# Performance work log

Hardware: AMD Instinct MI355X
Metric: run time of the kernel (lower is better)

The kernel has to match this reference:

```python
import jax, jax.numpy as jnp
import numpy as np
from jax import lax

B, J, I = 32, 48, 48          # batch, target len, source len
W = 2                          # target_window_size
CTX = 2 * W + 1                # 5
E, H = 128, 256                # embedding_size, hidden_units
VT, VS = 32000, 32000          # target / source vocab
S = 2 * J                      # HMM states (word + null)


def setup_inputs() -> dict:
    key = jax.random.key(0)
    ks = jax.random.split(key, 12)
    inp = {
        "target_embedding": jax.random.normal(ks[0], (VT, E), jnp.float32) * 0.02,
        "W_bridge": jax.random.normal(ks[1], (E * CTX, E), jnp.float32) * 0.02,
        "W_hidden": jax.random.normal(ks[2], (E, H), jnp.float32) * 0.02,
        "b_hidden": jnp.zeros((H,), jnp.float32),
        "W_vocab": jax.random.normal(ks[3], (H, VS), jnp.float32) * 0.02,
        "b_vocab": jnp.zeros((VS,), jnp.float32),
        "transition": jax.random.uniform(ks[4], (B, S, S), jnp.float32, 0.01, 1.0),
        "initial_transition": jax.random.uniform(ks[5], (B, S), jnp.float32, 0.01, 1.0),
        "targets_ctx": jax.random.randint(ks[6], (B, J * CTX), 0, VT, jnp.int32),
        "targets_ctx_null": jax.random.randint(ks[7], (B, J * CTX), 0, VT, jnp.int32),
        "sources": jax.random.randint(ks[8], (B, I), 0, VS, jnp.int32),
    }
    return inp


def _emission(emb, Wb, Wh, bh, Wv, bv, ctx_ids, sources):
    # embedding lookup + context reshape: [B, J*CTX, E] -> [B, J, CTX*E]
    x = emb[ctx_ids].reshape(ctx_ids.shape[0], -1, CTX * E)
    h = jnp.tanh(jnp.einsum('bjc,ce,eh->bjh', x, Wb, Wh) + bh)  # bridge+hidden
    probs = jax.nn.softmax(h @ Wv + bv, axis=-1)                # [B, J, VS]
    # per-example gather of source token columns -> [B, J, I]
    return jax.vmap(lambda p, s: p[:, s])(probs, sources)


def _forward_backward(pi, A, em):
    # pi [B,S], A [B,S,S], em [B,S,I]; scaled HMM forward-backward
    e = jnp.moveaxis(em, 2, 0)  # [I, B, S]
    a0 = pi * e[0]
    c0 = a0.sum(-1, keepdims=True)
    a0 = a0 / c0

    def fstep(a, ei):
        an = jnp.einsum('bs,bst->bt', a, A) * ei
        c = an.sum(-1, keepdims=True)
        an = an / c
        return an, (an, c)

    _, (alphas, cs) = lax.scan(fstep, a0, e[1:])
    alphas = jnp.concatenate([a0[None], alphas], 0)          # [I,B,S]
    cs = jnp.concatenate([c0[None], cs], 0)                  # [I,B,1]

    def bstep(b, inp):
        ei, ci = inp
        bn = jnp.einsum('bst,bt->bs', A, ei * b) / ci
        return bn, bn

    bI = jnp.ones_like(a0)
    _, betas_rev = lax.scan(bstep, bI, (e[1:][::-1], cs[1:][::-1]))
    betas = jnp.concatenate([betas_rev[::-1], bI[None]], 0)  # [I,B,S]

    gamma = alphas * betas                                   # state posteriors
    loglik = jnp.log(cs[..., 0]).sum(0)                      # [B]
    return jnp.moveaxis(gamma, 0, 2), loglik


def reference(target_embedding, W_bridge, W_hidden, b_hidden, W_vocab, b_vocab,
              transition, initial_transition, targets_ctx, targets_ctx_null, sources):
    em_word = _emission(target_embedding, W_bridge, W_hidden, b_hidden,
                        W_vocab, b_vocab, targets_ctx, sources)       # [B,J,I]
    em_null = _emission(target_embedding, W_bridge, W_hidden, b_hidden,
                        W_vocab, b_vocab, targets_ctx_null, sources)  # [B,J,I]
    emission = jnp.concatenate([em_word, em_null], axis=1)            # [B,2J,I]
    gamma, loglik = _forward_backward(initial_transition, transition, emission)
    return gamma, -loglik
```

## Files before the change

kernel.cpp:

```cpp
#include <hip/hip_runtime.h>
#include <hip/hip_bf16.h>

#define NB 32
#define NJ 48
#define NI 48
#define NCTX 5
#define NE 128
#define NH 256
#define NVS 32000
#define NS 96
#define NR 3072

typedef __attribute__((ext_vector_type(8))) short bf16x8;
typedef __attribute__((ext_vector_type(4))) float f32x4;

__device__ __forceinline__ unsigned short f2b(float f) {
  __hip_bfloat16 h = __float2bfloat16(f);
  return *reinterpret_cast<unsigned short*>(&h);
}
__device__ __forceinline__ float wave_sum(float v) {
  v += __shfl_xor(v, 1);
  v += __shfl_xor(v, 2);
  v += __shfl_xor(v, 4);
  v += __shfl_xor(v, 8);
  v += __shfl_xor(v, 16);
  v += __shfl_xor(v, 32);
  return v;
}
__device__ __forceinline__ void gload_lds16(const void* g, void* l) {
  __builtin_amdgcn_global_load_lds(
      (const __attribute__((address_space(1))) void*)g,
      (__attribute__((address_space(3))) void*)l, 16, 0, 0);
}

__global__ __launch_bounds__(256) void k_transpose(const float* __restrict__ Wv,
                                                   unsigned char* __restrict__ Wv8) {
  __shared__ float tile[64][65];
  int t = threadIdx.x;
  int v0 = blockIdx.x * 64, k0 = blockIdx.y * 64;
  {
    int kr = t >> 4, vq = t & 15;
#pragma unroll
    for (int it = 0; it < 4; ++it) {
      float4 v = *(const float4*)&Wv[(k0 + kr + 16 * it) * NVS + v0 + vq * 4];
      tile[kr + 16 * it][vq * 4 + 0] = v.x;
      tile[kr + 16 * it][vq * 4 + 1] = v.y;
      tile[kr + 16 * it][vq * 4 + 2] = v.z;
      tile[kr + 16 * it][vq * 4 + 3] = v.w;
    }
  }
  __syncthreads();
  {
    int vl = t >> 2, kq = t & 3;
    unsigned int q8[4];
#pragma unroll
    for (int d = 0; d < 4; ++d) {
      float f0 = tile[kq * 16 + d * 4 + 0][vl] * 64.0f;
      float f1 = tile[kq * 16 + d * 4 + 1][vl] * 64.0f;
      float f2 = tile[kq * 16 + d * 4 + 2][vl] * 64.0f;
      float f3 = tile[kq * 16 + d * 4 + 3][vl] * 64.0f;
      int w = __builtin_amdgcn_cvt_pk_fp8_f32(f0, f1, 0, false);
      w = __builtin_amdgcn_cvt_pk_fp8_f32(f2, f3, w, true);
      q8[d] = (unsigned int)w;
    }
    *(uint4*)&Wv8[(v0 + vl) * 256 + k0 + kq * 16] = *(uint4*)q8;
  }
}

__global__ __launch_bounds__(256) void k_t2b(const float* __restrict__ src,
                                             unsigned short* __restrict__ dst,
                                             int R, int C) {
  __shared__ float tile[64][65];
  int t = threadIdx.x;
  int r0 = blockIdx.x * 64, c0 = blockIdx.y * 64;
  {
    int rr = t >> 4, cq = t & 15;
#pragma unroll
    for (int it = 0; it < 4; ++it) {
      float4 v = *(const float4*)&src[(r0 + rr + 16 * it) * C + c0 + cq * 4];
      tile[rr + 16 * it][cq * 4 + 0] = v.x;
      tile[rr + 16 * it][cq * 4 + 1] = v.y;
      tile[rr + 16 * it][cq * 4 + 2] = v.z;
      tile[rr + 16 * it][cq * 4 + 3] = v.w;
    }
  }
  __syncthreads();
  {
    int cc = t >> 2, rq = t & 3;
    unsigned short pk[16];
#pragma unroll
    for (int q = 0; q < 16; ++q) pk[q] = f2b(tile[rq * 16 + q][cc]);
    *(uint4*)&dst[(c0 + cc) * R + r0 + rq * 16] = *(uint4*)&pk[0];
    *(uint4*)&dst[(c0 + cc) * R + r0 + rq * 16 + 8] = *(uint4*)&pk[8];
  }
}

__global__ __launch_bounds__(256) void k_xb(const float* __restrict__ emb,
                                            const unsigned short* __restrict__ Wbt,
                                            const int* __restrict__ tc, const int* __restrict__ tcn,
                                            unsigned short* __restrict__ xb) {
  __shared__ unsigned short Ax[64 * 72];
  __shared__ unsigned short Bw[128 * 72];
  __shared__ unsigned short xout[64 * 136];
  int t = threadIdx.x;
  int r0 = blockIdx.x * 64;
  int wave = t >> 6, lane = t & 63;
  int wm = wave >> 1, wn = wave & 1;
  int lg = lane >> 4, lr = lane & 15;
  int arow = t >> 2, aseg = t & 3;
  int r = r0 + arow;
  int half = r / 1536, rem = r % 1536, bb = rem / 48, jj = rem % 48;
  const int* ids = half ? tcn : tc;
  int brow = t >> 1, bseg = t & 1;

  f32x4 acc[2][4];
#pragma unroll
  for (int m = 0; m < 2; ++m)
#pragma unroll
    for (int n = 0; n < 4; ++n) acc[m][n] = (f32x4){0.f, 0.f, 0.f, 0.f};

  for (int step = 0; step < 10; ++step) {
    int k0 = step * 64;
    int p = k0 >> 7;
    int e0 = k0 & 127;
    {
      int id = ids[bb * 240 + jj * 5 + p];
      const float4* er = (const float4*)&emb[id * 128 + e0 + aseg * 16];
      unsigned short pk[16];
#pragma unroll
      for (int q = 0; q < 4; ++q) {
        float4 v = er[q];
        pk[q * 4 + 0] = f2b(v.x);
        pk[q * 4 + 1] = f2b(v.y);
        pk[q * 4 + 2] = f2b(v.z);
        pk[q * 4 + 3] = f2b(v.w);
      }
      *(uint4*)&Ax[arow * 72 + aseg * 16] = *(uint4*)&pk[0];
      *(uint4*)&Ax[arow * 72 + aseg * 16 + 8] = *(uint4*)&pk[8];
    }
    {
      const uint4* wp = (const uint4*)&Wbt[brow * 640 + k0 + bseg * 32];
      uint4* dp = (uint4*)&Bw[brow * 72 + bseg * 32];
      uint4 w0 = wp[0], w1 = wp[1], w2 = wp[2], w3 = wp[3];
      dp[0] = w0; dp[1] = w1; dp[2] = w2; dp[3] = w3;
    }
    __syncthreads();
#pragma unroll
    for (int kk = 0; kk < 2; ++kk) {
      bf16x8 a[2], b[4];
#pragma unroll
      for (int m = 0; m < 2; ++m)
        a[m] = *(const bf16x8*)&Ax[(wm * 32 + m * 16 + lr) * 72 + kk * 32 + lg * 8];
#pragma unroll
      for (int n = 0; n < 4; ++n)
        b[n] = *(const bf16x8*)&Bw[(wn * 64 + n * 16 + lr) * 72 + kk * 32 + lg * 8];
#pragma unroll
      for (int m = 0; m < 2; ++m)
#pragma unroll
        for (int n = 0; n < 4; ++n)
          acc[m][n] = __builtin_amdgcn_mfma_f32_16x16x32_bf16(a[m], b[n], acc[m][n], 0, 0, 0);
    }
    __syncthreads();
  }
#pragma unroll
  for (int m = 0; m < 2; ++m)
#pragma unroll
    for (int n = 0; n < 4; ++n)
#pragma unroll
      for (int g = 0; g < 4; ++g)
        xout[(wm * 32 + m * 16 + lg * 4 + g) * 136 + wn * 64 + n * 16 + lr] = f2b(acc[m][n][g]);
  __syncthreads();
  {
    int orow = t >> 2, os = t & 3;
#pragma unroll
    for (int i = 0; i < 4; ++i)
      ((uint4*)&xb[(r0 + orow) * 128])[os * 4 + i] = *(uint4*)&xout[orow * 136 + (os * 4 + i) * 8];
  }
}

__global__ __launch_bounds__(256) void k_h(const unsigned short* __restrict__ xb,
                                           const unsigned short* __restrict__ Wht,
                                           const float* __restrict__ bh,
                                           unsigned char* __restrict__ hb8) {
  __shared__ char smem[69632];
  unsigned short* Asm = (unsigned short*)smem;
  unsigned short* Bsm = (unsigned short*)(smem + 34816);
  unsigned char* o8 = (unsigned char*)smem;
  int t = threadIdx.x;
  int r0 = blockIdx.x * 128, n0 = blockIdx.y * 128;
  int wave = t >> 6, lane = t & 63;
  int wm = wave >> 1, wn = wave & 1;
  int lg = lane >> 4, lr = lane & 15;
  {
    int row = t >> 1, seg = t & 1;
#pragma unroll
    for (int i = 0; i < 8; ++i) {
      *(uint4*)&Asm[row * 136 + seg * 64 + i * 8] = *(const uint4*)&xb[(r0 + row) * 128 + seg * 64 + i * 8];
      *(uint4*)&Bsm[row * 136 + seg * 64 + i * 8] = *(const uint4*)&Wht[(n0 + row) * 128 + seg * 64 + i * 8];
    }
  }
  __syncthreads();
  f32x4 acc[4][4];
#pragma unroll
  for (int m = 0; m < 4; ++m)
#pragma unroll
    for (int n = 0; n < 4; ++n) acc[m][n] = (f32x4){0.f, 0.f, 0.f, 0.f};
#pragma unroll
  for (int kk = 0; kk < 4; ++kk) {
    bf16x8 a[4], b[4];
#pragma unroll
    for (int m = 0; m < 4; ++m)
      a[m] = *(const bf16x8*)&Asm[(wm * 64 + m * 16 + lr) * 136 + kk * 32 + lg * 8];
#pragma unroll
    for (int n = 0; n < 4; ++n)
      b[n] = *(const bf16x8*)&Bsm[(wn * 64 + n * 16 + lr) * 136 + kk * 32 + lg * 8];
#pragma unroll
    for (int m = 0; m < 4; ++m)
#pragma unroll
      for (int n = 0; n < 4; ++n)
        acc[m][n] = __builtin_amdgcn_mfma_f32_16x16x32_bf16(a[m], b[n], acc[m][n], 0, 0, 0);
  }
  __syncthreads();
#pragma unroll
  for (int n = 0; n < 4; ++n) {
    int cl = wn * 64 + n * 16 + lr;
    float bvv = bh[n0 + cl];
#pragma unroll
    for (int m = 0; m < 4; ++m) {
#pragma unroll
      for (int g = 0; g < 4; ++g) {
        int rl = wm * 64 + m * 16 + lg * 4 + g;
        float hv = tanhf(acc[m][n][g] + bvv);
        int p8 = __builtin_amdgcn_cvt_pk_fp8_f32(hv * 256.0f, 0.0f, 0, false);
        o8[rl * 144 + cl] = (unsigned char)(p8 & 0xFF);
      }
    }
  }
  __syncthreads();
  {
    int row = t >> 1, seg = t & 1;
#pragma unroll
    for (int i = 0; i < 4; ++i)
      *(uint4*)&hb8[(r0 + row) * 256 + n0 + seg * 64 + i * 16] = *(uint4*)&o8[row * 144 + seg * 64 + i * 16];
  }
}

__global__ __launch_bounds__(256) void k_denom(const unsigned char* __restrict__ hb8,
                                               const unsigned char* __restrict__ Wv8,
                                               const float* __restrict__ bv,
                                               float* __restrict__ dpart) {
  __shared__ __align__(16) char smem[65536];
  unsigned char* Asm = (unsigned char*)smem;
  unsigned char* Bsm = (unsigned char*)(smem + 32768);
  float* red2 = (float*)smem;
  int t = threadIdx.x;
  int bid = blockIdx.x;
  int xcd = bid & 7;
  int pos = bid >> 3;
  int tile = xcd * 750 + pos;
  int vt = tile / 24, rt = tile % 24;
  int v0 = vt * 128, r0 = rt * 128;
  int wave = t >> 6, lane = t & 63;
  int wm = wave >> 1, wn = wave & 1;
  int lg = lane >> 4, lr = lane & 15;

  {
    int rloc = lane >> 4;
    int seg = lane & 15;
#pragma unroll
    for (int c = 0; c < 8; ++c) {
      int chunk = wave * 8 + c;
      int row = chunk * 4 + rloc;
      int gseg = seg ^ (row & 15);
      gload_lds16(&hb8[(r0 + row) * 256 + gseg * 16], &Asm[chunk * 1024]);
      gload_lds16(&Wv8[(v0 + row) * 256 + gseg * 16], &Bsm[chunk * 1024]);
    }
  }
  __syncthreads();

  f32x4 acc[4][4];
#pragma unroll
  for (int m = 0; m < 4; ++m)
#pragma unroll
    for (int n = 0; n < 4; ++n) acc[m][n] = (f32x4){0.f, 0.f, 0.f, 0.f};

#pragma unroll
  for (int K = 0; K < 4; ++K) {
#pragma unroll
    for (int kk = 0; kk < 2; ++kk) {
      int lseg = (K << 2) + (kk << 1) + (lg >> 1);
      int hb = (lg & 1) << 3;
      long long a[4], b[4];
#pragma unroll
      for (int m = 0; m < 4; ++m) {
        int rr = wm * 64 + m * 16 + lr;
        a[m] = *(const long long*)&Asm[rr * 256 + ((lseg ^ lr) << 4) + hb];
      }
#pragma unroll
      for (int n = 0; n < 4; ++n) {
        int rr = wn * 64 + n * 16 + lr;
        b[n] = *(const long long*)&Bsm[rr * 256 + ((lseg ^ lr) << 4) + hb];
      }
#pragma unroll
      for (int m = 0; m < 4; ++m)
#pragma unroll
        for (int n = 0; n < 4; ++n)
          acc[m][n] = __builtin_amdgcn_mfma_f32_16x16x32_fp8_fp8(a[m], b[n], acc[m][n], 0, 0, 0);
    }
  }

  const float SC = 6.103515625e-05f;
  float rs[4][4];
#pragma unroll
  for (int m = 0; m < 4; ++m)
#pragma unroll
    for (int g = 0; g < 4; ++g) rs[m][g] = 0.f;
#pragma unroll
  for (int m = 0; m < 4; ++m) {
#pragma unroll
    for (int n = 0; n < 4; ++n) {
      float bvv = bv[v0 + wn * 64 + n * 16 + lr];
#pragma unroll
      for (int g = 0; g < 4; ++g) rs[m][g] += __expf(acc[m][n][g] * SC + bvv);
    }
  }
#pragma unroll
  for (int m = 0; m < 4; ++m)
#pragma unroll
    for (int g = 0; g < 4; ++g) {
      float v = rs[m][g];
      v += __shfl_xor(v, 1);
      v += __shfl_xor(v, 2);
      v += __shfl_xor(v, 4);
      v += __shfl_xor(v, 8);
      rs[m][g] = v;
    }
  __syncthreads();
  if (lr == 0) {
#pragma unroll
    for (int m = 0; m < 4; ++m)
#pragma unroll
      for (int g = 0; g < 4; ++g)
        red2[wn * 128 + wm * 64 + m * 16 + lg * 4 + g] = rs[m][g];
  }
  __syncthreads();
  if (t < 128) dpart[vt * NR + r0 + t] = red2[t] + red2[128 + t];
}

__global__ void k_reduce(const float* __restrict__ dpart, float* __restrict__ dsum) {
  int r = blockIdx.x * 256 + threadIdx.x;
  float s = 0.f;
  for (int vt = 0; vt < 250; ++vt) s += dpart[vt * NR + r];
  dsum[r] = s;
}

__global__ __launch_bounds__(64) void k_emis(const unsigned char* __restrict__ hb8,
                                             const unsigned char* __restrict__ Wv8,
                                             const float* __restrict__ bv,
                                             const float* __restrict__ dsum,
                                             const int* __restrict__ src,
                                             float* __restrict__ em) {
  __shared__ unsigned char A8[48 * 256];
  __shared__ unsigned char B8[48 * 256];
  int t = threadIdx.x;
  int bh = blockIdx.x;
  int b = bh & 31, half = bh >> 5;
  int row4 = t >> 4, seg = t & 15;
  int rbase = half * 1536 + b * 48;
#pragma unroll
  for (int c = 0; c < 12; ++c) {
    int row = c * 4 + row4;
    int gseg = seg ^ (row & 15);
    gload_lds16(&hb8[(rbase + row) * 256 + gseg * 16], &A8[c * 1024]);
    int sv = src[b * 48 + row];
    gload_lds16(&Wv8[sv * 256 + gseg * 16], &B8[c * 1024]);
  }
  __syncthreads();
  int lg = t >> 4, lr = t & 15;
  f32x4 acc[3][3];
#pragma unroll
  for (int m = 0; m < 3; ++m)
#pragma unroll
    for (int n = 0; n < 3; ++n) acc[m][n] = (f32x4){0.f, 0.f, 0.f, 0.f};
#pragma unroll
  for (int kk = 0; kk < 8; ++kk) {
    long long a[3], bb[3];
#pragma unroll
    for (int m = 0; m < 3; ++m) {
      int rr = m * 16 + lr;
      int off = rr * 256 + ((((kk << 1) | (lg >> 1)) ^ (rr & 15)) << 4) + ((lg & 1) << 3);
      a[m] = *(const long long*)&A8[off];
      bb[m] = *(const long long*)&B8[off];
    }
#pragma unroll
    for (int m = 0; m < 3; ++m)
#pragma unroll
      for (int n = 0; n < 3; ++n)
        acc[m][n] = __builtin_amdgcn_mfma_f32_16x16x32_fp8_fp8(a[m], bb[n], acc[m][n], 0, 0, 0);
  }
  const float SC = 6.103515625e-05f;
#pragma unroll
  for (int n = 0; n < 3; ++n) {
    int i = n * 16 + lr;
    int sv = src[b * 48 + i];
    float bvv = bv[sv];
#pragma unroll
    for (int m = 0; m < 3; ++m) {
#pragma unroll
      for (int g = 0; g < 4; ++g) {
        int j = m * 16 + lg * 4 + g;
        float val = __expf(acc[m][n][g] * SC + bvv) / dsum[rbase + j];
        em[b * 4608 + (half * 48 + j) * 48 + i] = val;
      }
    }
  }
}

__global__ __launch_bounds__(192) void k_fb(const float* __restrict__ Atr, const float* __restrict__ pi,
                                            const float* __restrict__ em, float* __restrict__ alph,
                                            float* __restrict__ betas, float* __restrict__ out1) {
  __shared__ float A_st[96 * 97];
  __shared__ float em_lds[48 * 97];
  __shared__ __align__(16) float vec_lds[96];
  __shared__ float red[3];
  int t = threadIdx.x;
  int bid = blockIdx.x;
  int b = bid & 31;
  int role = bid >> 5;
  int col = t >> 1, half = t & 1;
  int base = b * 4608;

  for (int idx = t; idx < 96 * 96; idx += 192) {
    int s = idx / 96, tt = idx % 96;
    A_st[s * 97 + tt] = Atr[b * 9216 + idx];
  }
  for (int idx = t; idx < 96 * 48; idx += 192) {
    int s = idx / 48, i = idx % 48;
    em_lds[i * 97 + s] = em[base + idx];
  }
  __syncthreads();

  float Areg[48];
  if (role == 0) {
#pragma unroll
    for (int ss = 0; ss < 48; ++ss) Areg[ss] = A_st[(half * 48 + ss) * 97 + col];

    float llsum;
    {
      float v = pi[b * 96 + col] * em_lds[0 * 97 + col];
      float ws = half ? 0.f : v;
      ws = wave_sum(ws);
      if ((t & 63) == 0) red[t >> 6] = ws;
      __syncthreads();
      float c = red[0] + red[1] + red[2];
      float a = v / c;
      if (!half) {
        vec_lds[col] = a;
        alph[base + col] = a;
      }
      llsum = logf(c);
      __syncthreads();
    }
    for (int i = 1; i < 48; ++i) {
      float p = 0.f;
      const float4* ap = (const float4*)&vec_lds[half * 48];
#pragma unroll
      for (int q = 0; q < 12; ++q) {
        float4 av = ap[q];
        p += av.x * Areg[4 * q] + av.y * Areg[4 * q + 1] + av.z * Areg[4 * q + 2] + av.w * Areg[4 * q + 3];
      }
      p += __shfl_xor(p, 1);
      float an = p * em_lds[i * 97 + col];
      float ws = half ? 0.f : an;
      ws = wave_sum(ws);
      if ((t & 63) == 0) red[t >> 6] = ws;
      __syncthreads();
      float c = red[0] + red[1] + red[2];
      float a = an / c;
      if (!half) {
        vec_lds[col] = a;
        alph[base + i * 96 + col] = a;
      }
      llsum += logf(c);
      __syncthreads();
    }
    if (t == 0) out1[b] = -llsum;
  } else {
#pragma unroll
    for (int tt = 0; tt < 48; ++tt) Areg[tt] = A_st[col * 97 + half * 48 + tt];

    if (!half) {
      betas[base + 47 * 96 + col] = 1.0f;
      vec_lds[col] = em_lds[47 * 97 + col];
    }
    __syncthreads();
    for (int i = 46; i >= 0; --i) {
      float p = 0.f;
      const float4* ep = (const float4*)&vec_lds[half * 48];
#pragma unroll
      for (int q = 0; q < 12; ++q) {
        float4 ev = ep[q];
        p += ev.x * Areg[4 * q] + ev.y * Areg[4 * q + 1] + ev.z * Areg[4 * q + 2] + ev.w * Areg[4 * q + 3];
      }
      p += __shfl_xor(p, 1);
      float ws = half ? 0.f : p;
      ws = wave_sum(ws);
      if ((t & 63) == 0) red[t >> 6] = ws;
      __syncthreads();
      float c = red[0] + red[1] + red[2];
      float bt = p / c;
      if (!half) {
        betas[base + i * 96 + col] = bt;
        vec_lds[col] = em_lds[i * 97 + col] * bt;
      }
      __syncthreads();
    }
  }
}

__global__ __launch_bounds__(128) void k_gamma(const float* __restrict__ alph,
                                               const float* __restrict__ betas,
                                               float* __restrict__ out0) {
  __shared__ float red[2];
  int b = blockIdx.x, i = blockIdx.y;
  int t = threadIdx.x;
  float g = 0.f;
  if (t < 96) g = alph[b * 4608 + i * 96 + t] * betas[b * 4608 + i * 96 + t];
  float ws = wave_sum(g);
  if ((t & 63) == 0) red[t >> 6] = ws;
  __syncthreads();
  float c = red[0] + red[1];
  if (t < 96) out0[b * 4608 + t * 48 + i] = g / c;
}

extern "C" void kernel_launch(void* const* d_in, const int* in_sizes, int n_in,
                              void* d_out, int out_size, void* d_ws, size_t ws_size,
                              hipStream_t stream) {
  const float* emb = (const float*)d_in[0];
  const float* Wb  = (const float*)d_in[1];
  const float* Wh  = (const float*)d_in[2];
  const float* bh  = (const float*)d_in[3];
  const float* Wv  = (const float*)d_in[4];
  const float* bv  = (const float*)d_in[5];
  const float* Atr = (const float*)d_in[6];
  const float* pi  = (const float*)d_in[7];
  const int* tc    = (const int*)d_in[8];
  const int* tcn   = (const int*)d_in[9];
  const int* src   = (const int*)d_in[10];

  float* out0 = (float*)d_out;
  float* out1 = out0 + NB * NS * NI;

  char* ws = (char*)d_ws;
  unsigned char* wv8 = (unsigned char*)(ws);
  unsigned char* hb8 = (unsigned char*)(ws + 8192000);
  float* dpart       = (float*)(ws + 8978432);
  float* betas       = (float*)(ws + 8978432);
  float* dsum        = (float*)(ws + 12050432);
  float* em          = (float*)(ws + 12062720);
  float* alph        = (float*)(ws + 12652544);
  unsigned short* wbt = (unsigned short*)(ws + 13242368);
  unsigned short* wht = (unsigned short*)(ws + 13406208);
  unsigned short* xb  = (unsigned short*)(ws + 13471744);

  k_transpose<<<dim3(500, 4), 256, 0, stream>>>(Wv, wv8);
  k_t2b<<<dim3(10, 2), 256, 0, stream>>>(Wb, wbt, 640, 128);
  k_t2b<<<dim3(2, 4), 256, 0, stream>>>(Wh, wht, 128, 256);
  k_xb<<<48, 256, 0, stream>>>(emb, wbt, tc, tcn, xb);
  k_h<<<dim3(24, 2), 256, 0, stream>>>(xb, wht, bh, hb8);
  k_denom<<<6000, 256, 0, stream>>>(hb8, wv8, bv, dpart);
  k_reduce<<<12, 256, 0, stream>>>(dpart, dsum);
  k_emis<<<64, 64, 0, stream>>>(hb8, wv8, bv, dsum, src, em);
  k_fb<<<64, 192, 0, stream>>>(Atr, pi, em, alph, betas, out1);
  k_gamma<<<dim3(32, 48), 128, 0, stream>>>(alph, betas, out0);
}
```

Measured before the change: 161.6 us.

## Double-buffer Wv tiles in k_denom covering two vocab tiles per block; shrink k_xb tiles

k_denom now has each block process two 128-column vocab tiles for one row tile. The A operand stays resident in LDS and the Wv operand streams in 64-byte K slices through a double buffer, with the next slice prefetched during MFMA work. The aim is to halve A reloads, cut LDS use for better occupancy, and overlap global loads with compute, at the cost of one barrier per K step. Separately, k_xb switches to 32-row tiles and twice as many blocks to spread the small GEMM over more CUs.

```diff
diff --git a/kernel.cpp b/kernel.cpp
--- a/kernel.cpp
+++ b/kernel.cpp
@@ -99,44 +99,36 @@
                                             const unsigned short* __restrict__ Wbt,
                                             const int* __restrict__ tc, const int* __restrict__ tcn,
                                             unsigned short* __restrict__ xb) {
-  __shared__ unsigned short Ax[64 * 72];
+  __shared__ unsigned short Ax[32 * 72];
   __shared__ unsigned short Bw[128 * 72];
-  __shared__ unsigned short xout[64 * 136];
-  int t = threadIdx.x;
-  int r0 = blockIdx.x * 64;
+  __shared__ unsigned short xout[32 * 136];
+  int t = threadIdx.x;
+  int r0 = blockIdx.x * 32;
   int wave = t >> 6, lane = t & 63;
   int wm = wave >> 1, wn = wave & 1;
   int lg = lane >> 4, lr = lane & 15;
-  int arow = t >> 2, aseg = t & 3;
+  int arow = t >> 3, aseg = t & 7;
   int r = r0 + arow;
   int half = r / 1536, rem = r % 1536, bb = rem / 48, jj = rem % 48;
   const int* ids = half ? tcn : tc;
   int brow = t >> 1, bseg = t & 1;
 
-  f32x4 acc[2][4];
-#pragma unroll
-  for (int m = 0; m < 2; ++m)
-#pragma unroll
-    for (int n = 0; n < 4; ++n) acc[m][n] = (f32x4){0.f, 0.f, 0.f, 0.f};
+  f32x4 acc[4];
+#pragma unroll
+  for (int n = 0; n < 4; ++n) acc[n] = (f32x4){0.f, 0.f, 0.f, 0.f};
 
   for (int step = 0; step < 10; ++step) {
     int k0 = step * 64;
-    int p = k0 >> 7;
-    int e0 = k0 & 127;
+    int p = step >> 1;
+    int e0 = (step & 1) * 64;
     {
       int id = ids[bb * 240 + jj * 5 + p];
-      const float4* er = (const float4*)&emb[id * 128 + e0 + aseg * 16];
-      unsigned short pk[16];
-#pragma unroll
-      for (int q = 0; q < 4; ++q) {
-        float4 v = er[q];
-        pk[q * 4 + 0] = f2b(v.x);
-        pk[q * 4 + 1] = f2b(v.y);
-        pk[q * 4 + 2] = f2b(v.z);
-        pk[q * 4 + 3] = f2b(v.w);
-      }
-      *(uint4*)&Ax[arow * 72 + aseg * 16] = *(uint4*)&pk[0];
-      *(uint4*)&Ax[arow * 72 + aseg * 16 + 8] = *(uint4*)&pk[8];
+      const float4* er = (const float4*)&emb[id * 128 + e0 + aseg * 8];
+      float4 v0 = er[0], v1 = er[1];
+      unsigned short pk[8];
+      pk[0] = f2b(v0.x); pk[1] = f2b(v0.y); pk[2] = f2b(v0.z); pk[3] = f2b(v0.w);
+      pk[4] = f2b(v1.x); pk[5] = f2b(v1.y); pk[6] = f2b(v1.z); pk[7] = f2b(v1.w);
+      *(uint4*)&Ax[arow * 72 + aseg * 8] = *(uint4*)&pk[0];
     }
     {
       const uint4* wp = (const uint4*)&Wbt[brow * 640 + k0 + bseg * 32];
@@ -147,34 +139,25 @@
     __syncthreads();
 #pragma unroll
     for (int kk = 0; kk < 2; ++kk) {
-      bf16x8 a[2], b[4];
-#pragma unroll
-      for (int m = 0; m < 2; ++m)
-        a[m] = *(const bf16x8*)&Ax[(wm * 32 + m * 16 + lr) * 72 + kk * 32 + lg * 8];
-#pragma unroll
-      for (int n = 0; n < 4; ++n)
-        b[n] = *(const bf16x8*)&Bw[(wn * 64 + n * 16 + lr) * 72 + kk * 32 + lg * 8];
-#pragma unroll
-      for (int m = 0; m < 2; ++m)
-#pragma unroll
-        for (int n = 0; n < 4; ++n)
-          acc[m][n] = __builtin_amdgcn_mfma_f32_16x16x32_bf16(a[m], b[n], acc[m][n], 0, 0, 0);
+      bf16x8 a = *(const bf16x8*)&Ax[(wm * 16 + lr) * 72 + kk * 32 + lg * 8];
+#pragma unroll
+      for (int n = 0; n < 4; ++n) {
+        bf16x8 b = *(const bf16x8*)&Bw[(wn * 64 + n * 16 + lr) * 72 + kk * 32 + lg * 8];
+        acc[n] = __builtin_amdgcn_mfma_f32_16x16x32_bf16(a, b, acc[n], 0, 0, 0);
+      }
     }
     __syncthreads();
   }
 #pragma unroll
-  for (int m = 0; m < 2; ++m)
-#pragma unroll
-    for (int n = 0; n < 4; ++n)
-#pragma unroll
-      for (int g = 0; g < 4; ++g)
-        xout[(wm * 32 + m * 16 + lg * 4 + g) * 136 + wn * 64 + n * 16 + lr] = f2b(acc[m][n][g]);
-  __syncthreads();
-  {
-    int orow = t >> 2, os = t & 3;
-#pragma unroll
-    for (int i = 0; i < 4; ++i)
-      ((uint4*)&xb[(r0 + orow) * 128])[os * 4 + i] = *(uint4*)&xout[orow * 136 + (os * 4 + i) * 8];
+  for (int n = 0; n < 4; ++n)
+#pragma unroll
+    for (int g = 0; g < 4; ++g)
+      xout[(wm * 16 + lg * 4 + g) * 136 + wn * 64 + n * 16 + lr] = f2b(acc[n][g]);
+  __syncthreads();
+  {
+    int orow = t >> 3, os = t & 7;
+    *(uint4*)&xb[(r0 + orow) * 128 + os * 16] = *(uint4*)&xout[orow * 136 + os * 16];
+    *(uint4*)&xb[(r0 + orow) * 128 + os * 16 + 8] = *(uint4*)&xout[orow * 136 + os * 16 + 8];
   }
 }
 
@@ -249,35 +232,41 @@
                                                const unsigned char* __restrict__ Wv8,
                                                const float* __restrict__ bv,
                                                float* __restrict__ dpart) {
-  __shared__ __align__(16) char smem[65536];
-  unsigned char* Asm = (unsigned char*)smem;
-  unsigned char* Bsm = (unsigned char*)(smem + 32768);
-  float* red2 = (float*)smem;
+  __shared__ __align__(16) unsigned char Asm[32768];
+  __shared__ __align__(16) unsigned char Bsm[2][8192];
+  __shared__ float red2[2][128];
   int t = threadIdx.x;
   int bid = blockIdx.x;
   int xcd = bid & 7;
   int pos = bid >> 3;
-  int tile = xcd * 750 + pos;
-  int vt = tile / 24, rt = tile % 24;
-  int v0 = vt * 128, r0 = rt * 128;
+  int tile = xcd * 375 + pos;
+  int vtp = tile / 24, rt = tile % 24;
+  int r0 = rt * 128;
   int wave = t >> 6, lane = t & 63;
   int wm = wave >> 1, wn = wave & 1;
   int lg = lane >> 4, lr = lane & 15;
 
   {
-    int rloc = lane >> 4;
-    int seg = lane & 15;
+    int rloc = lane >> 4, seg = lane & 15;
 #pragma unroll
     for (int c = 0; c < 8; ++c) {
       int chunk = wave * 8 + c;
       int row = chunk * 4 + rloc;
       int gseg = seg ^ (row & 15);
       gload_lds16(&hb8[(r0 + row) * 256 + gseg * 16], &Asm[chunk * 1024]);
-      gload_lds16(&Wv8[(v0 + row) * 256 + gseg * 16], &Bsm[chunk * 1024]);
-    }
-  }
-  __syncthreads();
-
+    }
+  }
+  int brloc = lane >> 2, bseg = lane & 3;
+#pragma unroll
+  for (int c = 0; c < 2; ++c) {
+    int i = wave * 2 + c;
+    int row = i * 16 + brloc;
+    int gseg = bseg ^ ((row >> 1) & 3);
+    gload_lds16(&Wv8[(vtp * 256 + row) * 256 + 0 * 64 + gseg * 16], &Bsm[0][i * 1024]);
+  }
+  __syncthreads();
+
+  const float SC = 6.103515625e-05f;
   f32x4 acc[4][4];
 #pragma unroll
   for (int m = 0; m < 4; ++m)
@@ -285,21 +274,35 @@
     for (int n = 0; n < 4; ++n) acc[m][n] = (f32x4){0.f, 0.f, 0.f, 0.f};
 
 #pragma unroll
-  for (int K = 0; K < 4; ++K) {
+  for (int step = 0; step < 8; ++step) {
+    int vt = step >> 2, ks = step & 3, buf = step & 1;
+    if (step < 7) {
+      int ns = step + 1;
+      int nvt = ns >> 2, nks = ns & 3, nbuf = ns & 1;
+#pragma unroll
+      for (int c = 0; c < 2; ++c) {
+        int i = wave * 2 + c;
+        int row = i * 16 + brloc;
+        int gseg = bseg ^ ((row >> 1) & 3);
+        gload_lds16(&Wv8[((vtp * 2 + nvt) * 128 + row) * 256 + nks * 64 + gseg * 16],
+                    &Bsm[nbuf][i * 1024]);
+      }
+    }
 #pragma unroll
     for (int kk = 0; kk < 2; ++kk) {
-      int lseg = (K << 2) + (kk << 1) + (lg >> 1);
+      int lsa = ks * 4 + kk * 2 + (lg >> 1);
+      int sb = kk * 2 + (lg >> 1);
       int hb = (lg & 1) << 3;
       long long a[4], b[4];
 #pragma unroll
       for (int m = 0; m < 4; ++m) {
         int rr = wm * 64 + m * 16 + lr;
-        a[m] = *(const long long*)&Asm[rr * 256 + ((lseg ^ lr) << 4) + hb];
+        a[m] = *(const long long*)&Asm[rr * 256 + ((lsa ^ lr) << 4) + hb];
       }
 #pragma unroll
       for (int n = 0; n < 4; ++n) {
         int rr = wn * 64 + n * 16 + lr;
-        b[n] = *(const long long*)&Bsm[rr * 256 + ((lseg ^ lr) << 4) + hb];
+        b[n] = *(const long long*)&Bsm[buf][rr * 64 + ((sb ^ ((rr >> 1) & 3)) << 4) + hb];
       }
 #pragma unroll
       for (int m = 0; m < 4; ++m)
@@ -307,44 +310,47 @@
         for (int n = 0; n < 4; ++n)
           acc[m][n] = __builtin_amdgcn_mfma_f32_16x16x32_fp8_fp8(a[m], b[n], acc[m][n], 0, 0, 0);
     }
-  }
-
-  const float SC = 6.103515625e-05f;
-  float rs[4][4];
-#pragma unroll
-  for (int m = 0; m < 4; ++m)
-#pragma unroll
-    for (int g = 0; g < 4; ++g) rs[m][g] = 0.f;
-#pragma unroll
-  for (int m = 0; m < 4; ++m) {
-#pragma unroll
-    for (int n = 0; n < 4; ++n) {
-      float bvv = bv[v0 + wn * 64 + n * 16 + lr];
-#pragma unroll
-      for (int g = 0; g < 4; ++g) rs[m][g] += __expf(acc[m][n][g] * SC + bvv);
-    }
-  }
-#pragma unroll
-  for (int m = 0; m < 4; ++m)
-#pragma unroll
-    for (int g = 0; g < 4; ++g) {
-      float v = rs[m][g];
-      v += __shfl_xor(v, 1);
-      v += __shfl_xor(v, 2);
-      v += __shfl_xor(v, 4);
-      v += __shfl_xor(v, 8);
-      rs[m][g] = v;
-    }
-  __syncthreads();
-  if (lr == 0) {
-#pragma unroll
-    for (int m = 0; m < 4; ++m)
-#pragma unroll
-      for (int g = 0; g < 4; ++g)
-        red2[wn * 128 + wm * 64 + m * 16 + lg * 4 + g] = rs[m][g];
-  }
-  __syncthreads();
-  if (t < 128) dpart[vt * NR + r0 + t] = red2[t] + red2[128 + t];
+    if (ks == 3) {
+      int v0 = (vtp * 2 + vt) * 128;
+      float rs[4][4];
+#pragma unroll
+      for (int m = 0; m < 4; ++m)
+#pragma unroll
+        for (int g = 0; g < 4; ++g) rs[m][g] = 0.f;
+#pragma unroll
+      for (int m = 0; m < 4; ++m) {
+#pragma unroll
+        for (int n = 0; n < 4; ++n) {
+          float bvv = bv[v0 + wn * 64 + n * 16 + lr];
+#pragma unroll
+          for (int g = 0; g < 4; ++g) rs[m][g] += __expf(acc[m][n][g] * SC + bvv);
+          acc[m][n] = (f32x4){0.f, 0.f, 0.f, 0.f};
+        }
+      }
+#pragma unroll
+      for (int m = 0; m < 4; ++m)
+#pragma unroll
+        for (int g = 0; g < 4; ++g) {
+          float v = rs[m][g];
+          v += __shfl_xor(v, 1);
+          v += __shfl_xor(v, 2);
+          v += __shfl_xor(v, 4);
+          v += __shfl_xor(v, 8);
+          rs[m][g] = v;
+        }
+      if (lr == 0) {
+#pragma unroll
+        for (int m = 0; m < 4; ++m)
+#pragma unroll
+          for (int g = 0; g < 4; ++g)
+            red2[wn][wm * 64 + m * 16 + lg * 4 + g] = rs[m][g];
+      }
+      __syncthreads();
+      if (t < 128) dpart[(vtp * 2 + vt) * NR + r0 + t] = red2[0][t] + red2[1][t];
+    } else {
+      __syncthreads();
+    }
+  }
 }
 
 __global__ void k_reduce(const float* __restrict__ dpart, float* __restrict__ dsum) {
@@ -566,9 +572,9 @@
   k_transpose<<<dim3(500, 4), 256, 0, stream>>>(Wv, wv8);
   k_t2b<<<dim3(10, 2), 256, 0, stream>>>(Wb, wbt, 640, 128);
   k_t2b<<<dim3(2, 4), 256, 0, stream>>>(Wh, wht, 128, 256);
-  k_xb<<<48, 256, 0, stream>>>(emb, wbt, tc, tcn, xb);
+  k_xb<<<96, 256, 0, stream>>>(emb, wbt, tc, tcn, xb);
   k_h<<<dim3(24, 2), 256, 0, stream>>>(xb, wht, bh, hb8);
-  k_denom<<<6000, 256, 0, stream>>>(hb8, wv8, bv, dpart);
+  k_denom<<<3000, 256, 0, stream>>>(hb8, wv8, bv, dpart);
   k_reduce<<<12, 256, 0, stream>>>(dpart, dsum);
   k_emis<<<64, 64, 0, stream>>>(hb8, wv8, bv, dsum, src, em);
   k_fb<<<64, 192, 0, stream>>>(Atr, pi, em, alph, betas, out1);
```

New measurement: 159.9 us. No clear change (-1.1%).
